# Kernel tuning notes

Measured on AMD Instinct MI355X. Metric: run time of the kernel, lower is better.

Reference implementation:

```python
import jax, jax.numpy as jnp
import numpy as np

B, S, D = 2, 2048, 1024
H, DK, DV = 16, 64, 64


def setup_inputs() -> dict:
    key = jax.random.key(0)
    ks = jax.random.split(key, 9)
    s = 0.02
    return {
        "x": jax.random.normal(ks[0], (B, S, D), dtype=jnp.float32),
        "mask": jnp.zeros((B, S), dtype=bool),  # True = padded position
        "Wq": jax.random.normal(ks[1], (D, H * DK), dtype=jnp.float32) * s,
        "bq": jnp.zeros((H * DK,), dtype=jnp.float32),
        "Wk": jax.random.normal(ks[2], (D, H * DK), dtype=jnp.float32) * s,
        "bk": jnp.zeros((H * DK,), dtype=jnp.float32),
        "Wv": jax.random.normal(ks[3], (D, H * DV), dtype=jnp.float32) * s,
        "bv": jnp.zeros((H * DV,), dtype=jnp.float32),
        "Wo": jax.random.normal(ks[4], (H * DV, D), dtype=jnp.float32) * s,
        "bo": jnp.zeros((D,), dtype=jnp.float32),
    }


def reference(x, mask, Wq, bq, Wk, bk, Wv, bv, Wo, bo):
    Bx, Sx, _ = x.shape
    # projections -> [B, H, S, dk/dv]
    q = (x @ Wq + bq).reshape(Bx, Sx, H, DK).transpose(0, 2, 1, 3)
    k = (x @ Wk + bk).reshape(Bx, Sx, H, DK).transpose(0, 2, 1, 3)
    v = (x @ Wv + bv).reshape(Bx, Sx, H, DV).transpose(0, 2, 1, 3)
    # scaled QK^T: [B, H, Sq, Sk]
    scores = jnp.einsum("bhqd,bhkd->bhqk", q, k) / jnp.sqrt(jnp.float32(DK))
    neg_inf = jnp.float32(-jnp.inf)
    # padding mask: True masks out key positions
    scores = jnp.where(mask[:, None, None, :], neg_inf, scores)
    # causal mask
    causal = jnp.triu(jnp.ones((Sx, Sx), dtype=bool), k=1)
    scores = jnp.where(causal[None, None, :, :], neg_inf, scores)
    attn = jax.nn.softmax(scores, axis=-1)
    out = jnp.einsum("bhqk,bhkd->bhqd", attn, v)  # [B, H, S, dv]
    out = out.transpose(0, 2, 1, 3).reshape(Bx, Sx, H * DV)
    return out @ Wo + bo
```

## Files before the change

kernel.cpp:

```cpp
#include <hip/hip_runtime.h>
#include <stdint.h>

typedef __bf16 bf16_t;
typedef __bf16 bf16x8 __attribute__((ext_vector_type(8)));
typedef float f32x4 __attribute__((ext_vector_type(4)));

#define S_LEN 2048
#define D_MODEL 1024
#define NH 16
#define DKV 64
#define BATCH 2

#define QSCALE 0.1803368801111204f

__device__ __forceinline__ uint16_t f2bfu(float f) {
    union { float f; uint32_t u; } c; c.f = f;
    return (uint16_t)((c.u + 0x7fffu + ((c.u >> 16) & 1u)) >> 16);
}
__device__ __forceinline__ bf16_t f2bf(float f) {
    union { uint16_t s; bf16_t b; } o; o.s = f2bfu(f);
    return o.b;
}
__device__ __forceinline__ uint32_t pack2t(float lo, float hi) {
    union { float f; uint32_t u; } a, b; a.f = lo; b.f = hi;
    return __builtin_amdgcn_perm(b.u, a.u, 0x07060302);
}
__device__ __forceinline__ void gld_lds16(const bf16_t* g, bf16_t* l) {
    __builtin_amdgcn_global_load_lds(
        (const __attribute__((address_space(1))) void*)g,
        (__attribute__((address_space(3))) void*)l, 16, 0, 0);
}

__global__ __launch_bounds__(256) void k_convert_x(const float* __restrict__ x,
                                                   bf16_t* __restrict__ xb, int n) {
    int i = (blockIdx.x * 256 + threadIdx.x) * 4;
    if (i < n) {
        float4 v = *(const float4*)(x + i);
        xb[i + 0] = f2bf(v.x);
        xb[i + 1] = f2bf(v.y);
        xb[i + 2] = f2bf(v.z);
        xb[i + 3] = f2bf(v.w);
    }
}

__global__ __launch_bounds__(256) void k_transpose4(
    const float* __restrict__ Wq, const float* __restrict__ Wk,
    const float* __restrict__ Wv, const float* __restrict__ Wo,
    bf16_t* __restrict__ WqkvT, bf16_t* __restrict__ WoT) {
    __shared__ float tile[64][65];
    int k0 = blockIdx.x * 64;
    int n0 = blockIdx.y * 64;
    const float* W; bf16_t* WT; int np, nw;
    if (n0 < 3072) {
        W = (n0 < 1024) ? Wq : (n0 < 2048) ? Wk : Wv;
        np = n0 & 1023; WT = WqkvT; nw = n0;
    } else {
        W = Wo; np = n0 - 3072; WT = WoT; nw = n0 - 3072;
    }
    int tx = threadIdx.x & 63, ty = threadIdx.x >> 6;
    #pragma unroll
    for (int r = ty; r < 64; r += 4)
        tile[r][tx] = W[(size_t)(k0 + r) * 1024 + np + tx];
    __syncthreads();
    #pragma unroll
    for (int r = ty; r < 64; r += 4)
        WT[(size_t)(nw + r) * 1024 + k0 + tx] = f2bf(tile[tx][r]);
}

#define BM 128
#define BN 128
#define BKK 64

__global__ __launch_bounds__(256) void k_gemm_qkv(
    const bf16_t* __restrict__ A, const bf16_t* __restrict__ BT, int K,
    const float* __restrict__ bias0, const float* __restrict__ bias1,
    const float* __restrict__ bias2,
    bf16_t* __restrict__ outQ, bf16_t* __restrict__ outK, bf16_t* __restrict__ outVt) {
    __shared__ __align__(16) bf16_t As[BM * BKK];
    __shared__ __align__(16) bf16_t Bs[BN * BKK];
    int m0 = blockIdx.x * BM;
    int n0 = blockIdx.y * BN;
    int t = threadIdx.x;
    int wid = t >> 6, lane = t & 63, l15 = lane & 15, quad = lane >> 4;
    int wr = (wid >> 1) * 64, wc = (wid & 1) * 64;
    int srow = t >> 3;
    int schunk = (t & 7) ^ (srow & 7);
    int sldst = (t & 7) * 8;
    const f32x4 fzero = {0.f, 0.f, 0.f, 0.f};
    f32x4 acc[4][4];
    #pragma unroll
    for (int i = 0; i < 4; i++)
        #pragma unroll
        for (int j = 0; j < 4; j++) acc[i][j] = fzero;

    int r7 = l15 & 7;
    for (int k0 = 0; k0 < K; k0 += BKK) {
        #pragma unroll
        for (int p = 0; p < 4; p++) {
            int r = p * 32 + srow;
            gld_lds16(&A[(size_t)(m0 + r) * K + k0 + schunk * 8], &As[r * 64 + sldst]);
            gld_lds16(&BT[(size_t)(n0 + r) * K + k0 + schunk * 8], &Bs[r * 64 + sldst]);
        }
        __syncthreads();
        #pragma unroll
        for (int kk = 0; kk < BKK; kk += 32) {
            int g = quad + (kk >> 3);
            int col = ((g ^ r7) << 3);
            bf16x8 af[4], bfr[4];
            #pragma unroll
            for (int mt = 0; mt < 4; mt++)
                af[mt] = *(const bf16x8*)&As[(wr + mt * 16 + l15) * 64 + col];
            #pragma unroll
            for (int nt = 0; nt < 4; nt++)
                bfr[nt] = *(const bf16x8*)&Bs[(wc + nt * 16 + l15) * 64 + col];
            #pragma unroll
            for (int mt = 0; mt < 4; mt++)
                #pragma unroll
                for (int nt = 0; nt < 4; nt++)
                    acc[mt][nt] = __builtin_amdgcn_mfma_f32_16x16x32_bf16(
                        af[mt], bfr[nt], acc[mt][nt], 0, 0, 0);
        }
        __syncthreads();
    }

    #pragma unroll
    for (int mt = 0; mt < 4; mt++) {
        #pragma unroll
        for (int nt = 0; nt < 4; nt++) {
            int gc = n0 + wc + nt * 16 + l15;
            int sec = gc >> 10;
            int nn = gc & 1023;
            int h = nn >> 6, d = nn & 63;
            int gr0 = m0 + wr + mt * 16 + quad * 4;
            int b = gr0 >> 11, s0 = gr0 & 2047;
            if (sec == 2) {
                float bv = bias2[nn];
                uint2 pk;
                pk.x = pack2t(acc[mt][nt][0] + bv, acc[mt][nt][1] + bv);
                pk.y = pack2t(acc[mt][nt][2] + bv, acc[mt][nt][3] + bv);
                *(uint2*)&outVt[(((size_t)(b * NH + h)) * DKV + d) * S_LEN + s0] = pk;
            } else {
                const float* bias = (sec == 0) ? bias0 : bias1;
                float bv = bias[nn];
                #pragma unroll
                for (int r = 0; r < 4; r++) {
                    float val = acc[mt][nt][r] + bv;
                    size_t idx = (((size_t)(b * NH + h)) * S_LEN + s0 + r) * DKV + d;
                    if (sec == 0) outQ[idx] = f2bf(val * QSCALE);
                    else          outK[idx] = f2bf(val);
                }
            }
        }
    }
}

__global__ __launch_bounds__(256) void k_gemm_out(
    const bf16_t* __restrict__ A, const bf16_t* __restrict__ BT, int N, int K,
    const float* __restrict__ bias, float* __restrict__ outF) {
    __shared__ __align__(16) bf16_t As[128 * 64];
    __shared__ __align__(16) bf16_t Bs[64 * 64];
    int m0 = blockIdx.x * 128;
    int n0 = blockIdx.y * 64;
    int t = threadIdx.x;
    int wid = t >> 6, lane = t & 63, l15 = lane & 15, quad = lane >> 4;
    int wr = wid * 32;
    int srow = t >> 3;
    int schunk = (t & 7) ^ (srow & 7);
    int sldst = (t & 7) * 8;
    const f32x4 fzero = {0.f, 0.f, 0.f, 0.f};
    f32x4 acc[2][4];
    #pragma unroll
    for (int i = 0; i < 2; i++)
        #pragma unroll
        for (int j = 0; j < 4; j++) acc[i][j] = fzero;

    int r7 = l15 & 7;
    for (int k0 = 0; k0 < K; k0 += 64) {
        #pragma unroll
        for (int p = 0; p < 4; p++) {
            int r = p * 32 + srow;
            gld_lds16(&A[(size_t)(m0 + r) * K + k0 + schunk * 8], &As[r * 64 + sldst]);
        }
        #pragma unroll
        for (int p = 0; p < 2; p++) {
            int r = p * 32 + srow;
            gld_lds16(&BT[(size_t)(n0 + r) * K + k0 + schunk * 8], &Bs[r * 64 + sldst]);
        }
        __syncthreads();
        #pragma unroll
        for (int kk = 0; kk < 64; kk += 32) {
            int g = quad + (kk >> 3);
            int col = ((g ^ r7) << 3);
            bf16x8 af[2], bfr[4];
            #pragma unroll
            for (int mt = 0; mt < 2; mt++)
                af[mt] = *(const bf16x8*)&As[(wr + mt * 16 + l15) * 64 + col];
            #pragma unroll
            for (int nt = 0; nt < 4; nt++)
                bfr[nt] = *(const bf16x8*)&Bs[(nt * 16 + l15) * 64 + col];
            #pragma unroll
            for (int mt = 0; mt < 2; mt++)
                #pragma unroll
                for (int nt = 0; nt < 4; nt++)
                    acc[mt][nt] = __builtin_amdgcn_mfma_f32_16x16x32_bf16(
                        af[mt], bfr[nt], acc[mt][nt], 0, 0, 0);
        }
        __syncthreads();
    }

    #pragma unroll
    for (int mt = 0; mt < 2; mt++) {
        #pragma unroll
        for (int nt = 0; nt < 4; nt++) {
            #pragma unroll
            for (int r = 0; r < 4; r++) {
                int gr = m0 + wr + mt * 16 + quad * 4 + r;
                int gc = n0 + nt * 16 + l15;
                outF[(size_t)gr * N + gc] = acc[mt][nt][r] + bias[gc];
            }
        }
    }
}

__global__ __launch_bounds__(256, 4) void k_attn10(
    const bf16_t* __restrict__ Q, const bf16_t* __restrict__ Kg,
    const bf16_t* __restrict__ Vt, const unsigned char* __restrict__ mask,
    bf16_t* __restrict__ O) {
    __shared__ __align__(16) bf16_t Ks0[64 * 64];
    __shared__ __align__(16) bf16_t Ks1[64 * 64];
    __shared__ __align__(16) bf16_t Vs0[64 * 64];
    __shared__ __align__(16) bf16_t Vs1[64 * 64];
    __shared__ __align__(16) bf16_t Ps[64 * 64];

    int bid = blockIdx.x;
    int bh = bid & 31;
    int u = bid >> 5;
    int a = u & 7, g2 = u >> 3;
    int qt = (g2 == 0) ? 31 - a : (g2 == 1) ? a : (g2 == 2) ? 23 - a : 8 + a;
    int b = bh >> 4, h = bh & 15;
    int t = threadIdx.x;
    int w = t >> 6, lane = t & 63, l15 = lane & 15, quad = lane >> 4;
    int r7 = l15 & 7;

    bool maskany;
    {
        const uint2* mrow = (const uint2*)&mask[b * S_LEN];
        uint2 m0 = mrow[lane], m1 = mrow[lane + 64];
        uint2 m2 = mrow[lane + 128], m3 = mrow[lane + 192];
        uint32_t mo = (m0.x | m0.y) | (m1.x | m1.y) | (m2.x | m2.y) | (m3.x | m3.y);
        maskany = __any(mo != 0);
    }

    const bf16_t* Qrow = Q + ((size_t)bh * S_LEN + qt * 64 + w * 16 + l15) * DKV;
    bf16x8 qf0 = *(const bf16x8*)&Qrow[quad * 8];
    bf16x8 qf1 = *(const bf16x8*)&Qrow[32 + quad * 8];

    const bf16_t* Kbh = Kg + (size_t)bh * S_LEN * DKV;
    const bf16_t* Vbh = Vt + (size_t)bh * DKV * S_LEN;

    const f32x4 fzero = {0.f, 0.f, 0.f, 0.f};
    f32x4 oacc[4];
    f32x4 lacc = fzero;
    #pragma unroll
    for (int nt = 0; nt < 4; nt++) oacc[nt] = fzero;

    const bf16_t one_b = (bf16_t)1.0f;
    const bf16x8 onesf = {one_b, one_b, one_b, one_b, one_b, one_b, one_b, one_b};

    int qg = qt * 64 + w * 16 + l15;

    int sr = t >> 3;
    int sc = (t & 7) ^ (sr & 7);
    int sl = (t & 7) * 8;

    #pragma unroll
    for (int p = 0; p < 2; p++) {
        int r = p * 32 + sr;
        gld_lds16(&Kbh[(size_t)r * DKV + sc * 8], &Ks0[r * 64 + sl]);
        gld_lds16(&Vbh[(size_t)r * S_LEN + sc * 8], &Vs0[r * 64 + sl]);
    }
    __syncthreads();

    auto TILE = [&](const bf16_t* __restrict__ Kr, const bf16_t* __restrict__ Vr,
                    bf16_t* __restrict__ Kw, bf16_t* __restrict__ Vw, int kt) {
        if (kt < qt) {
            int kb2 = (kt + 1) * 64;
            #pragma unroll
            for (int p = 0; p < 2; p++) {
                int r = p * 32 + sr;
                gld_lds16(&Kbh[(size_t)(kb2 + r) * DKV + sc * 8], &Kw[r * 64 + sl]);
                gld_lds16(&Vbh[(size_t)r * S_LEN + kb2 + sc * 8], &Vw[r * 64 + sl]);
            }
        }
        int kbase = kt * 64;

        f32x4 sacc[4];
        #pragma unroll
        for (int mt = 0; mt < 4; mt++) sacc[mt] = fzero;
        #pragma unroll
        for (int kk = 0; kk < 64; kk += 32) {
            bf16x8 qf = kk ? qf1 : qf0;
            int col = (((quad + (kk >> 3)) ^ r7) << 3);
            bf16x8 af[4];
            #pragma unroll
            for (int mt = 0; mt < 4; mt++)
                af[mt] = *(const bf16x8*)&Kr[(mt * 16 + l15) * 64 + col];
            __builtin_amdgcn_s_setprio(1);
            #pragma unroll
            for (int mt = 0; mt < 4; mt++)
                sacc[mt] = __builtin_amdgcn_mfma_f32_16x16x32_bf16(af[mt], qf, sacc[mt], 0, 0, 0);
            __builtin_amdgcn_s_setprio(0);
        }

        if (maskany) {
            #pragma unroll
            for (int mt = 0; mt < 4; mt++) {
                uint32_t mb = *(const uint32_t*)&mask[b * S_LEN + kbase + mt * 16 + quad * 4];
                #pragma unroll
                for (int r = 0; r < 4; r++)
                    sacc[mt][r] += (float)((mb >> (8 * r)) & 0xffu) * -1e30f;
            }
        }
        if (kt == qt) {
            #pragma unroll
            for (int mt = 0; mt < 4; mt++) {
                int kgb = kbase + mt * 16 + quad * 4;
                #pragma unroll
                for (int r = 0; r < 4; r++)
                    if (kgb + r > qg) sacc[mt][r] = -1e30f;
            }
        }
        #pragma unroll
        for (int mt = 0; mt < 4; mt++) {
            uint2 pk;
            pk.x = pack2t(exp2f(sacc[mt][0]), exp2f(sacc[mt][1]));
            pk.y = pack2t(exp2f(sacc[mt][2]), exp2f(sacc[mt][3]));
            int pc = (mt * 2 + (quad >> 1)) ^ r7;
            *(uint2*)&Ps[(w * 16 + l15) * 64 + pc * 8 + (quad & 1) * 4] = pk;
        }

        #pragma unroll
        for (int kk = 0; kk < 64; kk += 32) {
            bf16x8 pf = *(const bf16x8*)&Ps[(w * 16 + l15) * 64 +
                                             (((quad + (kk >> 3)) ^ r7) << 3)];
            int vcol = (((quad + (kk >> 3)) ^ r7) << 3);
            bf16x8 vf[4];
            #pragma unroll
            for (int nt = 0; nt < 4; nt++)
                vf[nt] = *(const bf16x8*)&Vr[(nt * 16 + l15) * 64 + vcol];
            __builtin_amdgcn_s_setprio(1);
            #pragma unroll
            for (int nt = 0; nt < 4; nt++)
                oacc[nt] = __builtin_amdgcn_mfma_f32_16x16x32_bf16(pf, vf[nt], oacc[nt], 0, 0, 0);
            lacc = __builtin_amdgcn_mfma_f32_16x16x32_bf16(pf, onesf, lacc, 0, 0, 0);
            __builtin_amdgcn_s_setprio(0);
        }

        if (kt < qt) __syncthreads();
    };

    for (int kt = 0; kt <= qt; kt += 2) {
        TILE(Ks0, Vs0, Ks1, Vs1, kt);
        if (kt + 1 <= qt) TILE(Ks1, Vs1, Ks0, Vs0, kt + 1);
    }

    #pragma unroll
    for (int r = 0; r < 4; r++) {
        float l = lacc[r];
        float invl = l > 0.f ? 1.f / l : 0.f;
        int q = qt * 64 + w * 16 + quad * 4 + r;
        #pragma unroll
        for (int nt = 0; nt < 4; nt++) {
            int d = nt * 16 + l15;
            O[((size_t)b * S_LEN + q) * D_MODEL + h * DKV + d] = f2bf(oacc[nt][r] * invl);
        }
    }
}

extern "C" void kernel_launch(void* const* d_in, const int* in_sizes, int n_in,
                              void* d_out, int out_size, void* d_ws, size_t ws_size,
                              hipStream_t stream) {
    const float* x = (const float*)d_in[0];
    const unsigned char* mask = (const unsigned char*)d_in[1];
    const float* Wq = (const float*)d_in[2];
    const float* bq = (const float*)d_in[3];
    const float* Wk = (const float*)d_in[4];
    const float* bk = (const float*)d_in[5];
    const float* Wv = (const float*)d_in[6];
    const float* bv = (const float*)d_in[7];
    const float* Wo = (const float*)d_in[8];
    const float* bo = (const float*)d_in[9];
    float* out = (float*)d_out;

    char* ws = (char*)d_ws;
    const size_t MB = 1024 * 1024;
    bf16_t* xb    = (bf16_t*)(ws + 0 * MB);
    bf16_t* WqkvT = (bf16_t*)(ws + 8 * MB);
    bf16_t* WoT   = (bf16_t*)(ws + 14 * MB);
    bf16_t* Qb    = (bf16_t*)(ws + 16 * MB);
    bf16_t* Kb    = (bf16_t*)(ws + 24 * MB);
    bf16_t* Vtb   = (bf16_t*)(ws + 32 * MB);
    bf16_t* AOb   = (bf16_t*)(ws + 40 * MB);

    k_convert_x<<<dim3(4096), dim3(256), 0, stream>>>(x, xb, 4 * 1024 * 1024);
    k_transpose4<<<dim3(16, 64), dim3(256), 0, stream>>>(Wq, Wk, Wv, Wo, WqkvT, WoT);
    k_gemm_qkv<<<dim3(32, 24), dim3(256), 0, stream>>>(
        xb, WqkvT, 1024, bq, bk, bv, Qb, Kb, Vtb);
    k_attn10<<<dim3(1024), dim3(256), 0, stream>>>(Qb, Kb, Vtb, mask, AOb);
    k_gemm_out<<<dim3(32, 16), dim3(256), 0, stream>>>(
        AOb, WoT, 1024, 1024, bo, out);
}
```

Before: 184.2 us.

## Merge prep kernels, stage V-transpose epilogue through LDS, use native exp2

Fuses the x-to-bf16 conversion and weight transpose into a single launch to save one kernel launch. In the QKV GEMM, V-section blocks now stage their transposed tile in shared memory and write 16-byte coalesced rows to Vt, replacing the scattered 8-byte stores. The attention softmax uses a raw v_exp_f32 instruction instead of exp2f, which drops the denormal/range handling and may change results for very negative inputs. The -1e30 mask values still flush to zero through the native exp.

```diff
diff --git a/kernel.cpp b/kernel.cpp
--- a/kernel.cpp
+++ b/kernel.cpp
@@ -25,31 +25,36 @@
     union { float f; uint32_t u; } a, b; a.f = lo; b.f = hi;
     return __builtin_amdgcn_perm(b.u, a.u, 0x07060302);
 }
+__device__ __forceinline__ float exp2_native(float x) {
+    float r;
+    asm("v_exp_f32 %0, %1" : "=v"(r) : "v"(x));
+    return r;
+}
 __device__ __forceinline__ void gld_lds16(const bf16_t* g, bf16_t* l) {
     __builtin_amdgcn_global_load_lds(
         (const __attribute__((address_space(1))) void*)g,
         (__attribute__((address_space(3))) void*)l, 16, 0, 0);
 }
 
-__global__ __launch_bounds__(256) void k_convert_x(const float* __restrict__ x,
-                                                   bf16_t* __restrict__ xb, int n) {
-    int i = (blockIdx.x * 256 + threadIdx.x) * 4;
-    if (i < n) {
+__global__ __launch_bounds__(256) void k_prep(
+    const float* __restrict__ x, bf16_t* __restrict__ xb,
+    const float* __restrict__ Wq, const float* __restrict__ Wk,
+    const float* __restrict__ Wv, const float* __restrict__ Wo,
+    bf16_t* __restrict__ WqkvT, bf16_t* __restrict__ WoT) {
+    __shared__ float tile[64][65];
+    int bid = blockIdx.x;
+    if (bid < 4096) {
+        int i = (bid * 256 + threadIdx.x) * 4;
         float4 v = *(const float4*)(x + i);
         xb[i + 0] = f2bf(v.x);
         xb[i + 1] = f2bf(v.y);
         xb[i + 2] = f2bf(v.z);
         xb[i + 3] = f2bf(v.w);
-    }
-}
-
-__global__ __launch_bounds__(256) void k_transpose4(
-    const float* __restrict__ Wq, const float* __restrict__ Wk,
-    const float* __restrict__ Wv, const float* __restrict__ Wo,
-    bf16_t* __restrict__ WqkvT, bf16_t* __restrict__ WoT) {
-    __shared__ float tile[64][65];
-    int k0 = blockIdx.x * 64;
-    int n0 = blockIdx.y * 64;
+        return;
+    }
+    int b2 = bid - 4096;
+    int k0 = (b2 & 15) * 64;
+    int n0 = (b2 >> 4) * 64;
     const float* W; bf16_t* WT; int np, nw;
     if (n0 < 3072) {
         W = (n0 < 1024) ? Wq : (n0 < 2048) ? Wk : Wv;
@@ -76,8 +81,9 @@
     const float* __restrict__ bias0, const float* __restrict__ bias1,
     const float* __restrict__ bias2,
     bf16_t* __restrict__ outQ, bf16_t* __restrict__ outK, bf16_t* __restrict__ outVt) {
-    __shared__ __align__(16) bf16_t As[BM * BKK];
-    __shared__ __align__(16) bf16_t Bs[BN * BKK];
+    __shared__ __align__(16) bf16_t smem[BM * BKK + BN * BKK];
+    bf16_t* const As = smem;
+    bf16_t* const Bs = smem + BM * BKK;
     int m0 = blockIdx.x * BM;
     int n0 = blockIdx.y * BN;
     int t = threadIdx.x;
@@ -123,32 +129,56 @@
         __syncthreads();
     }
 
+    int secb = n0 >> 10;
+    if (secb == 2) {
+        bf16_t* const Ct = smem;
+        int nbase = n0 & 1023;
+        #pragma unroll
+        for (int mt = 0; mt < 4; mt++) {
+            #pragma unroll
+            for (int nt = 0; nt < 4; nt++) {
+                int dl = wc + nt * 16 + l15;
+                float bv = bias2[nbase + dl];
+                int sl = wr + mt * 16 + quad * 4;
+                uint2 pk;
+                pk.x = pack2t(acc[mt][nt][0] + bv, acc[mt][nt][1] + bv);
+                pk.y = pack2t(acc[mt][nt][2] + bv, acc[mt][nt][3] + bv);
+                int c4 = (sl >> 2) ^ ((dl & 7) << 1);
+                *(uint2*)&Ct[dl * 128 + c4 * 4] = pk;
+            }
+        }
+        __syncthreads();
+        int b = m0 >> 11, sb = m0 & 2047;
+        #pragma unroll
+        for (int rr = 0; rr < 8; rr++) {
+            int row = rr * 16 + (t >> 4);
+            int s8 = t & 15;
+            int c4 = (s8 * 2) ^ ((row & 7) << 1);
+            uint4 vv = *(const uint4*)&Ct[row * 128 + c4 * 4];
+            int nn = nbase + row;
+            int h = nn >> 6, d = nn & 63;
+            *(uint4*)&outVt[(((size_t)(b * NH + h)) * DKV + d) * S_LEN + sb + s8 * 8] = vv;
+        }
+        return;
+    }
+
     #pragma unroll
     for (int mt = 0; mt < 4; mt++) {
         #pragma unroll
         for (int nt = 0; nt < 4; nt++) {
             int gc = n0 + wc + nt * 16 + l15;
-            int sec = gc >> 10;
             int nn = gc & 1023;
             int h = nn >> 6, d = nn & 63;
             int gr0 = m0 + wr + mt * 16 + quad * 4;
             int b = gr0 >> 11, s0 = gr0 & 2047;
-            if (sec == 2) {
-                float bv = bias2[nn];
-                uint2 pk;
-                pk.x = pack2t(acc[mt][nt][0] + bv, acc[mt][nt][1] + bv);
-                pk.y = pack2t(acc[mt][nt][2] + bv, acc[mt][nt][3] + bv);
-                *(uint2*)&outVt[(((size_t)(b * NH + h)) * DKV + d) * S_LEN + s0] = pk;
-            } else {
-                const float* bias = (sec == 0) ? bias0 : bias1;
-                float bv = bias[nn];
-                #pragma unroll
-                for (int r = 0; r < 4; r++) {
-                    float val = acc[mt][nt][r] + bv;
-                    size_t idx = (((size_t)(b * NH + h)) * S_LEN + s0 + r) * DKV + d;
-                    if (sec == 0) outQ[idx] = f2bf(val * QSCALE);
-                    else          outK[idx] = f2bf(val);
-                }
+            const float* bias = (secb == 0) ? bias0 : bias1;
+            float bv = bias[nn];
+            #pragma unroll
+            for (int r = 0; r < 4; r++) {
+                float val = acc[mt][nt][r] + bv;
+                size_t idx = (((size_t)(b * NH + h)) * S_LEN + s0 + r) * DKV + d;
+                if (secb == 0) outQ[idx] = f2bf(val * QSCALE);
+                else           outK[idx] = f2bf(val);
             }
         }
     }
@@ -222,7 +252,7 @@
     }
 }
 
-__global__ __launch_bounds__(256, 4) void k_attn10(
+__global__ __launch_bounds__(256, 4) void k_attn11(
     const bf16_t* __restrict__ Q, const bf16_t* __restrict__ Kg,
     const bf16_t* __restrict__ Vt, const unsigned char* __restrict__ mask,
     bf16_t* __restrict__ O) {
@@ -333,8 +363,8 @@
         #pragma unroll
         for (int mt = 0; mt < 4; mt++) {
             uint2 pk;
-            pk.x = pack2t(exp2f(sacc[mt][0]), exp2f(sacc[mt][1]));
-            pk.y = pack2t(exp2f(sacc[mt][2]), exp2f(sacc[mt][3]));
+            pk.x = pack2t(exp2_native(sacc[mt][0]), exp2_native(sacc[mt][1]));
+            pk.y = pack2t(exp2_native(sacc[mt][2]), exp2_native(sacc[mt][3]));
             int pc = (mt * 2 + (quad >> 1)) ^ r7;
             *(uint2*)&Ps[(w * 16 + l15) * 64 + pc * 8 + (quad & 1) * 4] = pk;
         }
@@ -402,11 +432,11 @@
     bf16_t* Vtb   = (bf16_t*)(ws + 32 * MB);
     bf16_t* AOb   = (bf16_t*)(ws + 40 * MB);
 
-    k_convert_x<<<dim3(4096), dim3(256), 0, stream>>>(x, xb, 4 * 1024 * 1024);
-    k_transpose4<<<dim3(16, 64), dim3(256), 0, stream>>>(Wq, Wk, Wv, Wo, WqkvT, WoT);
+    k_prep<<<dim3(4096 + 1024), dim3(256), 0, stream>>>(
+        x, xb, Wq, Wk, Wv, Wo, WqkvT, WoT);
     k_gemm_qkv<<<dim3(32, 24), dim3(256), 0, stream>>>(
         xb, WqkvT, 1024, bq, bk, bv, Qb, Kb, Vtb);
-    k_attn10<<<dim3(1024), dim3(256), 0, stream>>>(Qb, Kb, Vtb, mask, AOb);
+    k_attn11<<<dim3(1024), dim3(256), 0, stream>>>(Qb, Kb, Vtb, mask, AOb);
     k_gemm_out<<<dim3(32, 16), dim3(256), 0, stream>>>(
         AOb, WoT, 1024, 1024, bo, out);
 }
```

New measurement: 182.1 us. Within noise of the previous version (-1.1%).
